# Performance work log

Measured on AMD Instinct MI355X. Metric: run time of the kernel, lower is better.

## Reference

```python
import jax, jax.numpy as jnp
import numpy as np
from jax import lax

K = 5
C_IN, C_OUT, H, W, N = 256, 128, 270, 480, 512


def setup_inputs() -> dict:
    key = jax.random.key(0)
    ks = jax.random.split(key, 7)
    backbone_map = jax.random.normal(ks[0], (C_IN, H, W), dtype=jnp.float32)
    centers = jax.random.randint(ks[1], (N, 2), 0, 270, dtype=jnp.int32)
    L = jax.random.uniform(ks[2], (N, K), dtype=jnp.float32)
    conv_w = jax.random.normal(ks[3], (C_OUT, C_IN, 3, 3), dtype=jnp.float32) * 0.02
    conv_b = jax.random.normal(ks[4], (C_OUT,), dtype=jnp.float32) * 0.02
    fc_w = jax.random.normal(ks[5], (K, C_OUT), dtype=jnp.float32) * 0.05
    fc_b = jax.random.normal(ks[6], (K,), dtype=jnp.float32) * 0.05
    return {"backbone_map": backbone_map, "centers": centers, "L": L,
            "conv_w": conv_w, "conv_b": conv_b, "fc_w": fc_w, "fc_b": fc_b}


def reference(backbone_map, centers, L, conv_w, conv_b, fc_w, fc_b):
    # 3x3 conv, padding=1, 256 -> 128 channels (unbatched CHW input)
    x = backbone_map[None]  # [1, C_in, H, W]
    E = lax.conv_general_dilated(x, conv_w, window_strides=(1, 1), padding='SAME',
                                 dimension_numbers=('NCHW', 'OIHW', 'NCHW'))[0]
    E = jax.nn.relu(E + conv_b[:, None, None])  # [C_out, H, W]
    # per-object gather: vec_i = E[:, c_y, c_x]  (centers[i] = (c_x, c_y))
    c_x = centers[:, 0]
    c_y = centers[:, 1]
    vecs = E[:, c_y, c_x].T  # [N, C_out]
    logits = vecs @ fc_w.T + fc_b  # [N, K]
    P = jax.nn.softmax(logits, axis=-1)  # softmax over the K-vector per object
    L_identity = -jnp.sum(L * jnp.log(P))
    return P, L_identity
```

## Files before the change

kernel.cpp:

```cpp
#include <hip/hip_runtime.h>

#define C_IN   256
#define C_OUT  128
#define H_DIM  270
#define W_DIM  480
#define N_PTS  512
#define K_CLS  5

#define PB     16
#define CC     32
#define CI_PER (C_IN / CC)
#define TERMS  (CI_PER * 9)

__global__ __launch_bounds__(256) void gather_conv(
        const float* __restrict__ bb,
        const int*   __restrict__ centers,
        const float* __restrict__ conv_w,
        float*       __restrict__ part)
{
    __shared__ float patch[PB][TERMS];
    __shared__ float w_s[TERMS * C_OUT];

    const int chunk = blockIdx.x & (CC - 1);
    const int ptg   = blockIdx.x >> 5;
    const int t     = threadIdx.x;

    for (int i = t; i < PB * CI_PER * 3; i += 256) {
        const int pt  = i & 15;
        const int rem = i >> 4;
        const int lci = rem / 3;
        const int dy  = rem - lci * 3;
        const int n   = ptg * PB + pt;
        const int cx  = centers[2 * n];
        const int cy  = centers[2 * n + 1];
        const int y   = cy + dy - 1;
        float v0 = 0.f, v1 = 0.f, v2 = 0.f;
        if (y >= 0 && y < H_DIM) {
            const float* row = bb + ((size_t)(chunk * CI_PER + lci) * H_DIM + y)
                                  * W_DIM + cx;
            v1 = row[0];
            v2 = row[1];
            if (cx >= 1) v0 = row[-1];
        }
        float* dst = &patch[pt][lci * 9 + dy * 3];
        dst[0] = v0; dst[1] = v1; dst[2] = v2;
    }

    {
        const int co   = t >> 1;
        const int half = t & 1;
        const float* src = conv_w + (size_t)co * (C_IN * 9)
                                  + chunk * TERMS + half * (TERMS / 2);
        #pragma unroll
        for (int j = 0; j < TERMS / 8; ++j) {
            const float4 w4 = *(const float4*)(src + j * 4);
            const int T = half * (TERMS / 2) + j * 4;
            w_s[(T + 0) * C_OUT + co] = w4.x;
            w_s[(T + 1) * C_OUT + co] = w4.y;
            w_s[(T + 2) * C_OUT + co] = w4.z;
            w_s[(T + 3) * C_OUT + co] = w4.w;
        }
    }
    __syncthreads();

    const int cp = t & 63;
    const int q  = t >> 6;

    float acc[4][2] = {{0.f,0.f},{0.f,0.f},{0.f,0.f},{0.f,0.f}};

    for (int g = 0; g < TERMS; g += 4) {
        const float2 w0 = *(const float2*)&w_s[(g + 0) * C_OUT + 2 * cp];
        const float2 w1 = *(const float2*)&w_s[(g + 1) * C_OUT + 2 * cp];
        const float2 w2 = *(const float2*)&w_s[(g + 2) * C_OUT + 2 * cp];
        const float2 w3 = *(const float2*)&w_s[(g + 3) * C_OUT + 2 * cp];
        #pragma unroll
        for (int p = 0; p < 4; ++p) {
            const float4 pv = *(const float4*)&patch[q * 4 + p][g];
            acc[p][0] = fmaf(pv.x, w0.x, acc[p][0]);
            acc[p][1] = fmaf(pv.x, w0.y, acc[p][1]);
            acc[p][0] = fmaf(pv.y, w1.x, acc[p][0]);
            acc[p][1] = fmaf(pv.y, w1.y, acc[p][1]);
            acc[p][0] = fmaf(pv.z, w2.x, acc[p][0]);
            acc[p][1] = fmaf(pv.z, w2.y, acc[p][1]);
            acc[p][0] = fmaf(pv.w, w3.x, acc[p][0]);
            acc[p][1] = fmaf(pv.w, w3.y, acc[p][1]);
        }
    }

    float* pout = part + ((size_t)chunk * N_PTS + ptg * PB) * C_OUT + 2 * cp;
    #pragma unroll
    for (int p = 0; p < 4; ++p) {
        *(float2*)(pout + (size_t)(q * 4 + p) * C_OUT) =
            make_float2(acc[p][0], acc[p][1]);
    }
}

__global__ __launch_bounds__(64) void head_kernel(
        const float* __restrict__ part,
        const float* __restrict__ conv_b,
        const float* __restrict__ fc_w,
        const float* __restrict__ fc_b,
        const float* __restrict__ L,
        float*       __restrict__ P,
        float*       __restrict__ loss_part)
{
    const int n    = blockIdx.x;
    const int lane = threadIdx.x;

    const float* pc = part + (size_t)n * C_OUT;
    float v0 = 0.f, v1 = 0.f;
    #pragma unroll
    for (int c = 0; c < CC; ++c) {
        v0 += pc[(size_t)c * N_PTS * C_OUT + lane];
        v1 += pc[(size_t)c * N_PTS * C_OUT + 64 + lane];
    }
    v0 = fmaxf(v0 + conv_b[lane], 0.f);
    v1 = fmaxf(v1 + conv_b[64 + lane], 0.f);

    float logit[K_CLS];
    #pragma unroll
    for (int k = 0; k < K_CLS; ++k) {
        float p = v0 * fc_w[k * C_OUT + lane] + v1 * fc_w[k * C_OUT + 64 + lane];
        #pragma unroll
        for (int off = 32; off > 0; off >>= 1)
            p += __shfl_xor(p, off, 64);
        logit[k] = p + fc_b[k];
    }

    if (lane == 0) {
        float m = logit[0];
        #pragma unroll
        for (int k = 1; k < K_CLS; ++k) m = fmaxf(m, logit[k]);
        float e[K_CLS];
        float s = 0.f;
        #pragma unroll
        for (int k = 0; k < K_CLS; ++k) { e[k] = expf(logit[k] - m); s += e[k]; }
        const float inv  = 1.f / s;
        const float logs = logf(s);
        float lp = 0.f;
        #pragma unroll
        for (int k = 0; k < K_CLS; ++k) {
            P[n * K_CLS + k] = e[k] * inv;
            lp -= L[n * K_CLS + k] * ((logit[k] - m) - logs);
        }
        loss_part[n] = lp;
    }
}

__global__ __launch_bounds__(512) void reduce_loss(
        const float* __restrict__ loss_part, float* __restrict__ out) {
    __shared__ float sh[N_PTS];
    const int t = threadIdx.x;
    sh[t] = loss_part[t];
    __syncthreads();
    for (int s = N_PTS / 2; s > 0; s >>= 1) {
        if (t < s) sh[t] += sh[t + s];
        __syncthreads();
    }
    if (t == 0) out[0] = sh[0];
}

extern "C" void kernel_launch(void* const* d_in, const int* in_sizes, int n_in,
                              void* d_out, int out_size, void* d_ws, size_t ws_size,
                              hipStream_t stream) {
    const float* bb      = (const float*)d_in[0];
    const int*   centers = (const int*)  d_in[1];
    const float* L       = (const float*)d_in[2];
    const float* conv_w  = (const float*)d_in[3];
    const float* conv_b  = (const float*)d_in[4];
    const float* fc_w    = (const float*)d_in[5];
    const float* fc_b    = (const float*)d_in[6];

    float* out = (float*)d_out;

    float* part      = (float*)d_ws;
    float* loss_part = part + (size_t)CC * N_PTS * C_OUT;

    gather_conv<<<N_PTS / PB * CC, 256, 0, stream>>>(bb, centers, conv_w, part);
    head_kernel<<<N_PTS, 64, 0, stream>>>(part, conv_b, fc_w, fc_b, L, out, loss_part);
    reduce_loss<<<1, N_PTS, 0, stream>>>(loss_part, out + N_PTS * K_CLS);
}
```

Before: 25.73 us.

## Split input channels into 64 chunks and prefetch gathers and weights into registers

Templates the gather-conv kernel on the channel-chunk count and, when the workspace is large enough, splits the input channels into 64 chunks instead of 32. This doubles the block count and halves per-block work and shared memory. Global loads for the patch and weights are now issued into registers before any shared-memory stores, so the loads overlap. The head kernel reads partial sums and weights with float2 loads. The cost is twice as much partial-sum traffic for the head kernel to reduce, plus a runtime branch on workspace size.

Result: no change. 25.32 us (-1.6%).

```diff
diff --git a/kernel.cpp b/kernel.cpp
--- a/kernel.cpp
+++ b/kernel.cpp
@@ -6,60 +6,88 @@
 #define W_DIM  480
 #define N_PTS  512
 #define K_CLS  5
-
 #define PB     16
-#define CC     32
-#define CI_PER (C_IN / CC)
-#define TERMS  (CI_PER * 9)
-
+
+template<int CCT>
 __global__ __launch_bounds__(256) void gather_conv(
         const float* __restrict__ bb,
         const int*   __restrict__ centers,
         const float* __restrict__ conv_w,
         float*       __restrict__ part)
 {
+    constexpr int CI_PER = C_IN / CCT;
+    constexpr int TERMS  = CI_PER * 9;
+    constexpr int JOBS   = PB * CI_PER * 3;
+    constexpr int NJ     = (JOBS + 255) / 256;
+    constexpr int WPT    = TERMS / 2;
+
     __shared__ float patch[PB][TERMS];
     __shared__ float w_s[TERMS * C_OUT];
 
-    const int chunk = blockIdx.x & (CC - 1);
-    const int ptg   = blockIdx.x >> 5;
+    const int chunk = blockIdx.x % CCT;
+    const int ptg   = blockIdx.x / CCT;
     const int t     = threadIdx.x;
 
-    for (int i = t; i < PB * CI_PER * 3; i += 256) {
-        const int pt  = i & 15;
-        const int rem = i >> 4;
-        const int lci = rem / 3;
-        const int dy  = rem - lci * 3;
-        const int n   = ptg * PB + pt;
-        const int cx  = centers[2 * n];
-        const int cy  = centers[2 * n + 1];
-        const int y   = cy + dy - 1;
-        float v0 = 0.f, v1 = 0.f, v2 = 0.f;
-        if (y >= 0 && y < H_DIM) {
-            const float* row = bb + ((size_t)(chunk * CI_PER + lci) * H_DIM + y)
-                                  * W_DIM + cx;
-            v1 = row[0];
-            v2 = row[1];
-            if (cx >= 1) v0 = row[-1];
-        }
-        float* dst = &patch[pt][lci * 9 + dy * 3];
-        dst[0] = v0; dst[1] = v1; dst[2] = v2;
-    }
-
-    {
-        const int co   = t >> 1;
-        const int half = t & 1;
-        const float* src = conv_w + (size_t)co * (C_IN * 9)
-                                  + chunk * TERMS + half * (TERMS / 2);
-        #pragma unroll
-        for (int j = 0; j < TERMS / 8; ++j) {
-            const float4 w4 = *(const float4*)(src + j * 4);
-            const int T = half * (TERMS / 2) + j * 4;
-            w_s[(T + 0) * C_OUT + co] = w4.x;
-            w_s[(T + 1) * C_OUT + co] = w4.y;
-            w_s[(T + 2) * C_OUT + co] = w4.z;
-            w_s[(T + 3) * C_OUT + co] = w4.w;
-        }
+    float pv[NJ][3];
+    #pragma unroll
+    for (int jj = 0; jj < NJ; ++jj) {
+        pv[jj][0] = pv[jj][1] = pv[jj][2] = 0.f;
+        const int i = t + jj * 256;
+        if (i < JOBS) {
+            const int pt  = i & 15;
+            const int rem = i >> 4;
+            const int lci = rem / 3;
+            const int dy  = rem - lci * 3;
+            const int n   = ptg * PB + pt;
+            const int cx  = centers[2 * n];
+            const int cy  = centers[2 * n + 1];
+            const int y   = cy + dy - 1;
+            if (y >= 0 && y < H_DIM) {
+                const float* row = bb +
+                    ((size_t)(chunk * CI_PER + lci) * H_DIM + y) * W_DIM + cx;
+                pv[jj][1] = row[0];
+                pv[jj][2] = row[1];
+                if (cx >= 1) pv[jj][0] = row[-1];
+            }
+        }
+    }
+
+    const int co   = t >> 1;
+    const int half = t & 1;
+    const float* wsrc = conv_w + (size_t)co * (C_IN * 9)
+                              + chunk * TERMS + half * WPT;
+    float4 wreg[WPT / 4];
+    #pragma unroll
+    for (int j = 0; j < WPT / 4; ++j)
+        wreg[j] = *(const float4*)(wsrc + j * 4);
+    float2 wtail = make_float2(0.f, 0.f);
+    if constexpr ((WPT & 3) != 0)
+        wtail = *(const float2*)(wsrc + (WPT / 4) * 4);
+
+    #pragma unroll
+    for (int jj = 0; jj < NJ; ++jj) {
+        const int i = t + jj * 256;
+        if (i < JOBS) {
+            const int pt  = i & 15;
+            const int rem = i >> 4;
+            const int lci = rem / 3;
+            const int dy  = rem - lci * 3;
+            float* dst = &patch[pt][lci * 9 + dy * 3];
+            dst[0] = pv[jj][0]; dst[1] = pv[jj][1]; dst[2] = pv[jj][2];
+        }
+    }
+    #pragma unroll
+    for (int j = 0; j < WPT / 4; ++j) {
+        const int T = half * WPT + j * 4;
+        w_s[(T + 0) * C_OUT + co] = wreg[j].x;
+        w_s[(T + 1) * C_OUT + co] = wreg[j].y;
+        w_s[(T + 2) * C_OUT + co] = wreg[j].z;
+        w_s[(T + 3) * C_OUT + co] = wreg[j].w;
+    }
+    if constexpr ((WPT & 3) != 0) {
+        const int T = half * WPT + (WPT / 4) * 4;
+        w_s[(T + 0) * C_OUT + co] = wtail.x;
+        w_s[(T + 1) * C_OUT + co] = wtail.y;
     }
     __syncthreads();
 
@@ -75,15 +103,15 @@
         const float2 w3 = *(const float2*)&w_s[(g + 3) * C_OUT + 2 * cp];
         #pragma unroll
         for (int p = 0; p < 4; ++p) {
-            const float4 pv = *(const float4*)&patch[q * 4 + p][g];
-            acc[p][0] = fmaf(pv.x, w0.x, acc[p][0]);
-            acc[p][1] = fmaf(pv.x, w0.y, acc[p][1]);
-            acc[p][0] = fmaf(pv.y, w1.x, acc[p][0]);
-            acc[p][1] = fmaf(pv.y, w1.y, acc[p][1]);
-            acc[p][0] = fmaf(pv.z, w2.x, acc[p][0]);
-            acc[p][1] = fmaf(pv.z, w2.y, acc[p][1]);
-            acc[p][0] = fmaf(pv.w, w3.x, acc[p][0]);
-            acc[p][1] = fmaf(pv.w, w3.y, acc[p][1]);
+            const float4 pvv = *(const float4*)&patch[q * 4 + p][g];
+            acc[p][0] = fmaf(pvv.x, w0.x, acc[p][0]);
+            acc[p][1] = fmaf(pvv.x, w0.y, acc[p][1]);
+            acc[p][0] = fmaf(pvv.y, w1.x, acc[p][0]);
+            acc[p][1] = fmaf(pvv.y, w1.y, acc[p][1]);
+            acc[p][0] = fmaf(pvv.z, w2.x, acc[p][0]);
+            acc[p][1] = fmaf(pvv.z, w2.y, acc[p][1]);
+            acc[p][0] = fmaf(pvv.w, w3.x, acc[p][0]);
+            acc[p][1] = fmaf(pvv.w, w3.y, acc[p][1]);
         }
     }
 
@@ -95,6 +123,7 @@
     }
 }
 
+template<int CCT>
 __global__ __launch_bounds__(64) void head_kernel(
         const float* __restrict__ part,
         const float* __restrict__ conv_b,
@@ -107,20 +136,22 @@
     const int n    = blockIdx.x;
     const int lane = threadIdx.x;
 
-    const float* pc = part + (size_t)n * C_OUT;
-    float v0 = 0.f, v1 = 0.f;
-    #pragma unroll
-    for (int c = 0; c < CC; ++c) {
-        v0 += pc[(size_t)c * N_PTS * C_OUT + lane];
-        v1 += pc[(size_t)c * N_PTS * C_OUT + 64 + lane];
-    }
-    v0 = fmaxf(v0 + conv_b[lane], 0.f);
-    v1 = fmaxf(v1 + conv_b[64 + lane], 0.f);
+    const float* pc = part + (size_t)n * C_OUT + 2 * lane;
+    float vx = 0.f, vy = 0.f;
+    #pragma unroll
+    for (int c = 0; c < CCT; ++c) {
+        const float2 p = *(const float2*)(pc + (size_t)c * N_PTS * C_OUT);
+        vx += p.x; vy += p.y;
+    }
+    const float2 cb = *(const float2*)&conv_b[2 * lane];
+    vx = fmaxf(vx + cb.x, 0.f);
+    vy = fmaxf(vy + cb.y, 0.f);
 
     float logit[K_CLS];
     #pragma unroll
     for (int k = 0; k < K_CLS; ++k) {
-        float p = v0 * fc_w[k * C_OUT + lane] + v1 * fc_w[k * C_OUT + 64 + lane];
+        const float2 w = *(const float2*)&fc_w[k * C_OUT + 2 * lane];
+        float p = vx * w.x + vy * w.y;
         #pragma unroll
         for (int off = 32; off > 0; off >>= 1)
             p += __shfl_xor(p, off, 64);
@@ -172,11 +203,22 @@
     const float* fc_b    = (const float*)d_in[6];
 
     float* out = (float*)d_out;
-
-    float* part      = (float*)d_ws;
-    float* loss_part = part + (size_t)CC * N_PTS * C_OUT;
-
-    gather_conv<<<N_PTS / PB * CC, 256, 0, stream>>>(bb, centers, conv_w, part);
-    head_kernel<<<N_PTS, 64, 0, stream>>>(part, conv_b, fc_w, fc_b, L, out, loss_part);
-    reduce_loss<<<1, N_PTS, 0, stream>>>(loss_part, out + N_PTS * K_CLS);
-}
+    float* part = (float*)d_ws;
+
+    const size_t need64 = ((size_t)64 * N_PTS * C_OUT + N_PTS) * sizeof(float);
+    if (ws_size >= need64) {
+        float* loss_part = part + (size_t)64 * N_PTS * C_OUT;
+        gather_conv<64><<<(N_PTS / PB) * 64, 256, 0, stream>>>(
+            bb, centers, conv_w, part);
+        head_kernel<64><<<N_PTS, 64, 0, stream>>>(
+            part, conv_b, fc_w, fc_b, L, out, loss_part);
+        reduce_loss<<<1, N_PTS, 0, stream>>>(loss_part, out + N_PTS * K_CLS);
+    } else {
+        float* loss_part = part + (size_t)32 * N_PTS * C_OUT;
+        gather_conv<32><<<(N_PTS / PB) * 32, 256, 0, stream>>>(
+            bb, centers, conv_w, part);
+        head_kernel<32><<<N_PTS, 64, 0, stream>>>(
+            part, conv_b, fc_w, fc_b, L, out, loss_part);
+        reduce_loss<<<1, N_PTS, 0, stream>>>(loss_part, out + N_PTS * K_CLS);
+    }
+}
```
